# Performance work log

Measured on AMD Instinct MI355X. Metric: run time of the kernel, lower is better.

## Reference

```python
import jax, jax.numpy as jnp
import numpy as np

B, S, D_IN, D_H, D_OUT = 8, 4096, 512, 1024, 512


def setup_inputs() -> dict:
    key = jax.random.key(0)
    ks = jax.random.split(key, 7)
    # scale weights by 1/sqrt(fan_in) so activations stay O(1) through the ReLU stack
    return {
        "query": jax.random.normal(ks[0], (B, S, D_IN), dtype=jnp.float32),
        "W0": jax.random.normal(ks[1], (B, D_H, D_IN), dtype=jnp.float32) * (D_IN ** -0.5),
        "b0": jax.random.normal(ks[2], (B, D_H), dtype=jnp.float32) * 0.02,
        "W1": jax.random.normal(ks[3], (B, D_H, D_H), dtype=jnp.float32) * (D_H ** -0.5),
        "b1": jax.random.normal(ks[4], (B, D_H), dtype=jnp.float32) * 0.02,
        "W2": jax.random.normal(ks[5], (B, D_OUT, D_H), dtype=jnp.float32) * (D_H ** -0.5),
        "b2": jax.random.normal(ks[6], (B, D_OUT), dtype=jnp.float32) * 0.02,
    }


def reference(query, W0, b0, W1, b1, W2, b2):
    # Original loops over (seq, batch) issuing F.linear per sample with per-batch
    # weights; this is exactly a batched GEMM over the batch axis.
    # F.linear(x, w, b) = x @ w.T + b, with w[b] of shape [out, in].
    h = jax.nn.relu(jnp.einsum('bsd,bhd->bsh', query, W0) + b0[:, None, :])  # [B,S,H]
    h = jax.nn.relu(jnp.einsum('bsh,bgh->bsg', h, W1) + b1[:, None, :])      # [B,S,H]
    out = jnp.einsum('bsg,bog->bso', h, W2) + b2[:, None, :]                 # [B,S,O]
    return out
```

## Files before the change

### kernel.cpp

```cpp
#include <hip/hip_runtime.h>


typedef _Float16 f16x8 __attribute__((ext_vector_type(8)));
typedef _Float16 f16x4 __attribute__((ext_vector_type(4)));
typedef float    f32x4 __attribute__((ext_vector_type(4)));

__global__ __launch_bounds__(256) void cast_f32_f16(const float* __restrict__ src,
                                                    _Float16* __restrict__ dst,
                                                    int n4) {
    int i = blockIdx.x * 256 + threadIdx.x;
    const int stride = gridDim.x * 256;
    for (; i < n4; i += stride) {
        float4 f = reinterpret_cast<const float4*>(src)[i];
        f16x4 o;
        o[0] = (_Float16)f.x; o[1] = (_Float16)f.y;
        o[2] = (_Float16)f.z; o[3] = (_Float16)f.w;
        reinterpret_cast<f16x4*>(dst)[i] = o;
    }
}

template <bool SRC_F16>
__device__ __forceinline__ uint4 load8(const char* p) {
    if constexpr (SRC_F16) {
        return *reinterpret_cast<const uint4*>(p);
    } else {
        const float4* fp = reinterpret_cast<const float4*>(p);
        float4 f0 = fp[0], f1 = fp[1];
        f16x8 o;
        o[0] = (_Float16)f0.x; o[1] = (_Float16)f0.y;
        o[2] = (_Float16)f0.z; o[3] = (_Float16)f0.w;
        o[4] = (_Float16)f1.x; o[5] = (_Float16)f1.y;
        o[6] = (_Float16)f1.z; o[7] = (_Float16)f1.w;
        return __builtin_bit_cast(uint4, o);
    }
}

template <bool A_F16, bool W_F16, bool RELU, bool OUT_F16>
__global__ __launch_bounds__(256) void gemm_bias_act(
    const void* __restrict__ Av, const void* __restrict__ Wv,
    const float* __restrict__ bias, void* __restrict__ Outv,
    int M, int N, int K) {
    constexpr int BM = 128, BN = 128, BK = 32;
    __shared__ __align__(16) _Float16 As[BM * BK];
    __shared__ __align__(16) _Float16 Bs[BN * BK];

    const int tid  = threadIdx.x;
    const int lane = tid & 63;
    const int wave = tid >> 6;
    const int rowl = lane & 15;
    const int q    = lane >> 4;
    const int q8   = q * 8;
    const int wm   = (wave >> 1) * 64;
    const int wn   = (wave & 1) * 64;

    const int bm = blockIdx.x, bn = blockIdx.y, b = blockIdx.z;

    const int c0 = tid, c1 = tid + 256;
    const int ar0 = c0 >> 2, ak0 = (c0 & 3) * 8;
    const int ar1 = c1 >> 2, ak1 = (c1 & 3) * 8;

    constexpr size_t esA = A_F16 ? 2 : 4;
    constexpr size_t esW = W_F16 ? 2 : 4;
    const char* Abase = (const char*)Av;
    const char* Wbase = (const char*)Wv;

    size_t aoff0 = ((size_t)b * M * K + (size_t)(bm * BM + ar0) * K + ak0) * esA;
    size_t aoff1 = ((size_t)b * M * K + (size_t)(bm * BM + ar1) * K + ak1) * esA;
    size_t woff0 = ((size_t)b * N * K + (size_t)(bn * BN + ar0) * K + ak0) * esW;
    size_t woff1 = ((size_t)b * N * K + (size_t)(bn * BN + ar1) * K + ak1) * esW;

    f32x4 acc[4][4];
#pragma unroll
    for (int mi = 0; mi < 4; ++mi)
#pragma unroll
        for (int ni = 0; ni < 4; ++ni)
            acc[mi][ni] = (f32x4){0.f, 0.f, 0.f, 0.f};

    const int nk = K / BK;
    for (int kk = 0; kk < nk; ++kk) {
        uint4 va0 = load8<A_F16>(Abase + aoff0);
        uint4 va1 = load8<A_F16>(Abase + aoff1);
        uint4 vw0 = load8<W_F16>(Wbase + woff0);
        uint4 vw1 = load8<W_F16>(Wbase + woff1);
        aoff0 += BK * esA; aoff1 += BK * esA;
        woff0 += BK * esW; woff1 += BK * esW;

        __syncthreads();
        *(uint4*)(As + ar0 * BK + ak0) = va0;
        *(uint4*)(As + ar1 * BK + ak1) = va1;
        *(uint4*)(Bs + ar0 * BK + ak0) = vw0;
        *(uint4*)(Bs + ar1 * BK + ak1) = vw1;
        __syncthreads();

        f16x8 af[4], bf[4];
#pragma unroll
        for (int i = 0; i < 4; ++i)
            af[i] = *(const f16x8*)(As + (wm + i * 16 + rowl) * BK + q8);
#pragma unroll
        for (int i = 0; i < 4; ++i)
            bf[i] = *(const f16x8*)(Bs + (wn + i * 16 + rowl) * BK + q8);
#pragma unroll
        for (int mi = 0; mi < 4; ++mi)
#pragma unroll
            for (int ni = 0; ni < 4; ++ni)
                acc[mi][ni] = __builtin_amdgcn_mfma_f32_16x16x32_f16(
                    af[mi], bf[ni], acc[mi][ni], 0, 0, 0);
    }

    float bcol[4];
    {
        const float* bp = bias + (size_t)b * N + bn * BN + wn;
#pragma unroll
        for (int ni = 0; ni < 4; ++ni) bcol[ni] = bp[ni * 16 + rowl];
    }
#pragma unroll
    for (int mi = 0; mi < 4; ++mi) {
        const int row0 = bm * BM + wm + mi * 16 + q * 4;
#pragma unroll
        for (int r = 0; r < 4; ++r) {
            const size_t ro = (size_t)b * M * N + (size_t)(row0 + r) * N + bn * BN + wn;
#pragma unroll
            for (int ni = 0; ni < 4; ++ni) {
                float v = acc[mi][ni][r] + bcol[ni];
                if (RELU) v = fmaxf(v, 0.f);
                if (OUT_F16)
                    ((_Float16*)Outv)[ro + ni * 16 + rowl] = (_Float16)v;
                else
                    ((float*)Outv)[ro + ni * 16 + rowl] = v;
            }
        }
    }
}

extern "C" void kernel_launch(void* const* d_in, const int* in_sizes, int n_in,
                              void* d_out, int out_size, void* d_ws, size_t ws_size,
                              hipStream_t stream) {
    const int B = 8, S = 4096, DI = 512, DH = 1024, DO = 512;
    const float* query = (const float*)d_in[0];
    const float* W0    = (const float*)d_in[1];
    const float* b0    = (const float*)d_in[2];
    const float* W1    = (const float*)d_in[3];
    const float* b1    = (const float*)d_in[4];
    const float* W2    = (const float*)d_in[5];
    const float* b2    = (const float*)d_in[6];

    char* ws = (char*)d_ws;
    const size_t nH  = (size_t)B * S * DH;
    const size_t nQ  = (size_t)B * S * DI;
    const size_t nW0 = (size_t)B * DH * DI;
    const size_t nW1 = (size_t)B * DH * DH;
    const size_t nW2 = (size_t)B * DO * DH;

    _Float16* h0 = (_Float16*)ws;
    _Float16* h1 = (_Float16*)(ws + nH * 2);
    const size_t off_casts = nH * 4;
    const size_t full_need = off_casts + (nQ + nW0 + nW1 + nW2) * 2;

    const dim3 blk(256);
    const dim3 g0(S / 128, DH / 128, B);
    const dim3 g2(S / 128, DO / 128, B);

    if (ws_size >= full_need) {
        _Float16* qf  = (_Float16*)(ws + off_casts);
        _Float16* w0f = qf + nQ;
        _Float16* w1f = w0f + nW0;
        _Float16* w2f = w1f + nW1;
        cast_f32_f16<<<dim3(1024), blk, 0, stream>>>(query, qf,  (int)(nQ / 4));
        cast_f32_f16<<<dim3(1024), blk, 0, stream>>>(W0,    w0f, (int)(nW0 / 4));
        cast_f32_f16<<<dim3(1024), blk, 0, stream>>>(W1,    w1f, (int)(nW1 / 4));
        cast_f32_f16<<<dim3(1024), blk, 0, stream>>>(W2,    w2f, (int)(nW2 / 4));
        gemm_bias_act<true, true, true,  true ><<<g0, blk, 0, stream>>>(qf, w0f, b0, h0, S, DH, DI);
        gemm_bias_act<true, true, true,  true ><<<g0, blk, 0, stream>>>(h0, w1f, b1, h1, S, DH, DH);
        gemm_bias_act<true, true, false, false><<<g2, blk, 0, stream>>>(h1, w2f, b2, d_out, S, DO, DH);
    } else {
        gemm_bias_act<false, false, true,  true ><<<g0, blk, 0, stream>>>(query, W0, b0, h0, S, DH, DI);
        gemm_bias_act<true,  false, true,  true ><<<g0, blk, 0, stream>>>(h0, W1, b1, h1, S, DH, DH);
        gemm_bias_act<true,  false, false, false><<<g2, blk, 0, stream>>>(h1, W2, b2, d_out, S, DO, DH);
    }
}
```

Measured before the change: 389.5 us.

## Stage f16 GEMM tiles via direct global-to-LDS loads and merge cast kernels

When an operand is already f16, the GEMM now copies tiles straight from global memory into LDS with global_load_lds, skipping the round trip through registers. The four separate f32-to-f16 cast launches are merged into one kernel with a larger grid, which removes launch overhead. The LDS layout stays compatible because each thread's 16-byte chunk lands at offset 8*c, matching the earlier row*BK+k indexing. The loads are now issued after the first barrier instead of before it, so global latency is no longer hidden behind the previous tile's wait.

```diff
diff --git a/kernel.cpp b/kernel.cpp
--- a/kernel.cpp
+++ b/kernel.cpp
@@ -5,34 +5,45 @@
 typedef _Float16 f16x4 __attribute__((ext_vector_type(4)));
 typedef float    f32x4 __attribute__((ext_vector_type(4)));
 
-__global__ __launch_bounds__(256) void cast_f32_f16(const float* __restrict__ src,
-                                                    _Float16* __restrict__ dst,
-                                                    int n4) {
-    int i = blockIdx.x * 256 + threadIdx.x;
+__device__ __forceinline__ void stage16(const void* g, void* l) {
+    __builtin_amdgcn_global_load_lds(
+        (const __attribute__((address_space(1))) unsigned int*)g,
+        (__attribute__((address_space(3))) unsigned int*)l,
+        16, 0, 0);
+}
+
+__device__ __forceinline__ void cast_seg(const float* __restrict__ s,
+                                         _Float16* __restrict__ d, int n4) {
     const int stride = gridDim.x * 256;
-    for (; i < n4; i += stride) {
-        float4 f = reinterpret_cast<const float4*>(src)[i];
+    for (int i = blockIdx.x * 256 + threadIdx.x; i < n4; i += stride) {
+        float4 f = reinterpret_cast<const float4*>(s)[i];
         f16x4 o;
         o[0] = (_Float16)f.x; o[1] = (_Float16)f.y;
         o[2] = (_Float16)f.z; o[3] = (_Float16)f.w;
-        reinterpret_cast<f16x4*>(dst)[i] = o;
+        reinterpret_cast<f16x4*>(d)[i] = o;
     }
 }
 
-template <bool SRC_F16>
-__device__ __forceinline__ uint4 load8(const char* p) {
-    if constexpr (SRC_F16) {
-        return *reinterpret_cast<const uint4*>(p);
-    } else {
-        const float4* fp = reinterpret_cast<const float4*>(p);
-        float4 f0 = fp[0], f1 = fp[1];
-        f16x8 o;
-        o[0] = (_Float16)f0.x; o[1] = (_Float16)f0.y;
-        o[2] = (_Float16)f0.z; o[3] = (_Float16)f0.w;
-        o[4] = (_Float16)f1.x; o[5] = (_Float16)f1.y;
-        o[6] = (_Float16)f1.z; o[7] = (_Float16)f1.w;
-        return __builtin_bit_cast(uint4, o);
-    }
+__global__ __launch_bounds__(256) void cast_all(
+    const float* s0, _Float16* d0, int n0,
+    const float* s1, _Float16* d1, int n1,
+    const float* s2, _Float16* d2, int n2,
+    const float* s3, _Float16* d3, int n3) {
+    cast_seg(s0, d0, n0);
+    cast_seg(s1, d1, n1);
+    cast_seg(s2, d2, n2);
+    cast_seg(s3, d3, n3);
+}
+
+__device__ __forceinline__ uint4 load8f32(const char* p) {
+    const float4* fp = reinterpret_cast<const float4*>(p);
+    float4 f0 = fp[0], f1 = fp[1];
+    f16x8 o;
+    o[0] = (_Float16)f0.x; o[1] = (_Float16)f0.y;
+    o[2] = (_Float16)f0.z; o[3] = (_Float16)f0.w;
+    o[4] = (_Float16)f1.x; o[5] = (_Float16)f1.y;
+    o[6] = (_Float16)f1.z; o[7] = (_Float16)f1.w;
+    return __builtin_bit_cast(uint4, o);
 }
 
 template <bool A_F16, bool W_F16, bool RELU, bool OUT_F16>
@@ -46,12 +57,10 @@
 
     const int tid  = threadIdx.x;
     const int lane = tid & 63;
-    const int wave = tid >> 6;
     const int rowl = lane & 15;
-    const int q    = lane >> 4;
-    const int q8   = q * 8;
-    const int wm   = (wave >> 1) * 64;
-    const int wn   = (wave & 1) * 64;
+    const int q8   = (lane >> 4) * 8;
+    const int wm   = ((tid >> 6) >> 1) * 64;
+    const int wn   = ((tid >> 6) & 1) * 64;
 
     const int bm = blockIdx.x, bn = blockIdx.y, b = blockIdx.z;
 
@@ -78,18 +87,27 @@
 
     const int nk = K / BK;
     for (int kk = 0; kk < nk; ++kk) {
-        uint4 va0 = load8<A_F16>(Abase + aoff0);
-        uint4 va1 = load8<A_F16>(Abase + aoff1);
-        uint4 vw0 = load8<W_F16>(Wbase + woff0);
-        uint4 vw1 = load8<W_F16>(Wbase + woff1);
+        uint4 va0, va1, vw0, vw1;
+        if (!A_F16) { va0 = load8f32(Abase + aoff0); va1 = load8f32(Abase + aoff1); }
+        if (!W_F16) { vw0 = load8f32(Wbase + woff0); vw1 = load8f32(Wbase + woff1); }
+
+        __syncthreads();
+        if (A_F16) {
+            stage16(Abase + aoff0, As + 8 * (size_t)c0);
+            stage16(Abase + aoff1, As + 8 * (size_t)c1);
+        } else {
+            *(uint4*)(As + ar0 * BK + ak0) = va0;
+            *(uint4*)(As + ar1 * BK + ak1) = va1;
+        }
+        if (W_F16) {
+            stage16(Wbase + woff0, Bs + 8 * (size_t)c0);
+            stage16(Wbase + woff1, Bs + 8 * (size_t)c1);
+        } else {
+            *(uint4*)(Bs + ar0 * BK + ak0) = vw0;
+            *(uint4*)(Bs + ar1 * BK + ak1) = vw1;
+        }
         aoff0 += BK * esA; aoff1 += BK * esA;
         woff0 += BK * esW; woff1 += BK * esW;
-
-        __syncthreads();
-        *(uint4*)(As + ar0 * BK + ak0) = va0;
-        *(uint4*)(As + ar1 * BK + ak1) = va1;
-        *(uint4*)(Bs + ar0 * BK + ak0) = vw0;
-        *(uint4*)(Bs + ar1 * BK + ak1) = vw1;
         __syncthreads();
 
         f16x8 af[4], bf[4];
@@ -107,6 +125,7 @@
                     af[mi], bf[ni], acc[mi][ni], 0, 0, 0);
     }
 
+    const int q = lane >> 4;
     float bcol[4];
     {
         const float* bp = bias + (size_t)b * N + bn * BN + wn;
@@ -165,10 +184,9 @@
         _Float16* w0f = qf + nQ;
         _Float16* w1f = w0f + nW0;
         _Float16* w2f = w1f + nW1;
-        cast_f32_f16<<<dim3(1024), blk, 0, stream>>>(query, qf,  (int)(nQ / 4));
-        cast_f32_f16<<<dim3(1024), blk, 0, stream>>>(W0,    w0f, (int)(nW0 / 4));
-        cast_f32_f16<<<dim3(1024), blk, 0, stream>>>(W1,    w1f, (int)(nW1 / 4));
-        cast_f32_f16<<<dim3(1024), blk, 0, stream>>>(W2,    w2f, (int)(nW2 / 4));
+        cast_all<<<dim3(2048), blk, 0, stream>>>(
+            query, qf, (int)(nQ / 4), W0, w0f, (int)(nW0 / 4),
+            W1, w1f, (int)(nW1 / 4), W2, w2f, (int)(nW2 / 4));
         gemm_bias_act<true, true, true,  true ><<<g0, blk, 0, stream>>>(qf, w0f, b0, h0, S, DH, DI);
         gemm_bias_act<true, true, true,  true ><<<g0, blk, 0, stream>>>(h0, w1f, b1, h1, S, DH, DH);
         gemm_bias_act<true, true, false, false><<<g2, blk, 0, stream>>>(h1, w2f, b2, d_out, S, DO, DH);
```

Result: no change. 382.1 us (-1.9%).
